# Optimization experiments

Hardware: AMD Instinct MI355X
Metric: run time of the kernel (lower is better)

The kernel has to match this reference:

```python
import jax, jax.numpy as jnp
import numpy as np

B, T, C, H, D, G, V, M = 4, 1024, 768, 12, 4, 4, 32000, 1024
S = C // H


def layernorm(x, g, b, eps=1e-5):
    mu = jnp.mean(x, -1, keepdims=True)
    var = jnp.mean(jnp.square(x - mu), -1, keepdims=True)
    return (x - mu) * jax.lax.rsqrt(var + eps) * g + b


def setup_inputs() -> dict:
    key = jax.random.key(0)
    ks = jax.random.split(key, 12)
    std = 0.02  # matches _init_weights normal(0, 0.02)
    n = lambda k, sh: jax.random.normal(k, sh, jnp.float32) * std
    return {
        'x': jax.random.randint(ks[0], (B, T), 0, V),
        'y': jax.random.randint(ks[1], (B, T), 0, V),
        'wordemb': n(ks[2], (V, C)),
        'posemb': n(ks[3], (M, C)),
        'Wq': n(ks[4], (D, C, C)),
        'Wk': n(ks[5], (D, C, C)),
        'Wv': n(ks[6], (D, C, C)),
        'Wo': n(ks[7], (D, C, C)),
        'bo': jnp.zeros((D, C), jnp.float32),
        'ln1_g': jnp.ones((D, C), jnp.float32),
        'ln1_b': jnp.zeros((D, C), jnp.float32),
        'W1': n(ks[8], (D, C, G * C)),
        'b1': jnp.zeros((D, G * C), jnp.float32),
        'W2': n(ks[9], (D, G * C, C)),
        'b2': jnp.zeros((D, C), jnp.float32),
        'ln2_g': jnp.ones((D, C), jnp.float32),
        'ln2_b': jnp.zeros((D, C), jnp.float32),
        'Wl': n(ks[10], (C, V)),
        'bl': jnp.zeros((V,), jnp.float32),
    }


def _forward(x, y, wordemb, posemb, Wq, Wk, Wv, Wo, bo, ln1_g, ln1_b,
             W1, b1, W2, b2, ln2_g, ln2_b, Wl, bl):
    b, t = x.shape
    emb = wordemb[x] + posemb[:t][None, :, :]  # (b,t,c)
    causal = jnp.tril(jnp.ones((t, t), bool))

    def block(h_in, p):
        wq, wk, wv, wo, bo_, g1, be1, w1, b1_, w2, b2_, g2, be2 = p
        q = (h_in @ wq).reshape(b, t, H, S)
        k = (h_in @ wk).reshape(b, t, H, S)
        v = (h_in @ wv).reshape(b, t, H, S)
        # note: original scales by sqrt(channels), NOT sqrt(head_dim)
        w = jnp.einsum('bqhs,bkhs->bhqk', q, k) / jnp.sqrt(jnp.float32(C))
        w = jnp.where(causal, w, -jnp.inf)
        w = jax.nn.softmax(w, axis=-1)
        att = jnp.einsum('bhqk,bkhs->bqhs', w, v).reshape(b, t, C)
        att = att @ wo + bo_
        h1 = h_in + layernorm(att, g1, be1)   # x + norm1(attn(x))
        ff = jax.nn.relu(h1 @ w1 + b1_) @ w2 + b2_
        h2 = h1 + layernorm(ff, g2, be2)      # x + norm2(ff(x)); dropout=0
        return h2, None

    hfin, _ = jax.lax.scan(
        block, emb,
        (Wq, Wk, Wv, Wo, bo, ln1_g, ln1_b, W1, b1, W2, b2, ln2_g, ln2_b))
    logits = hfin @ Wl + bl  # (b,t,v)
    logp = jax.nn.log_softmax(logits, axis=-1)
    nll = -jnp.take_along_axis(logp, y[..., None], axis=-1)[..., 0]
    loss = jnp.mean(nll)
    return logits, loss


def reference(x, y, wordemb, posemb, Wq, Wk, Wv, Wo, bo, ln1_g, ln1_b,
              W1, b1, W2, b2, ln2_g, ln2_b, Wl, bl):
    return _forward(x, y, wordemb, posemb, Wq, Wk, Wv, Wo, bo, ln1_g, ln1_b,
                    W1, b1, W2, b2, ln2_g, ln2_b, Wl, bl)
```

## Files before the change

kernel.cpp:

```cpp
#include <hip/hip_runtime.h>

#define Bn 4
#define Tn 1024
#define Cn 768
#define Hn 12
#define Dn 4
#define Vn 32000
#define BTn (Bn*Tn)
#define NBX 125

typedef __attribute__((ext_vector_type(8))) short short8;
typedef __attribute__((ext_vector_type(4))) float f32x4;

__device__ __forceinline__ unsigned short f2bf(float f) {
  union { float f; unsigned u; } v; v.f = f;
  unsigned r = v.u + 0x7fffu + ((v.u >> 16) & 1u);
  return (unsigned short)(r >> 16);
}
__device__ __forceinline__ float bf2f(unsigned short us) {
  union { unsigned u; float f; } t; t.u = ((unsigned)us) << 16; return t.f;
}

__device__ __forceinline__ void gload_lds16(const void* g, void* l) {
  __builtin_amdgcn_global_load_lds(
      (const __attribute__((address_space(1))) void*)g,
      (__attribute__((address_space(3))) void*)l, 16, 0, 0);
}

__global__ __launch_bounds__(256)
void transpose_bf16_kernel(const float* __restrict__ src0, unsigned short* __restrict__ dst0,
                           int K, int N, size_t sStride, size_t dStride) {
  const float* src = src0 + blockIdx.z * sStride;
  unsigned short* dst = dst0 + blockIdx.z * dStride;
  __shared__ float tile[32][33];
  const int tx = threadIdx.x, ty = threadIdx.y;
  const int n0 = blockIdx.x * 32, k0 = blockIdx.y * 32;
#pragma unroll
  for (int i = 0; i < 4; ++i)
    tile[ty + i*8][tx] = src[(size_t)(k0 + ty + i*8) * N + n0 + tx];
  __syncthreads();
#pragma unroll
  for (int i = 0; i < 4; ++i)
    dst[(size_t)(n0 + ty + i*8) * K + k0 + tx] = f2bf(tile[tx][ty + i*8]);
}

__global__ __launch_bounds__(256)
void embed_kernel(const int* __restrict__ x, const float* __restrict__ wordemb,
                  const float* __restrict__ posemb, unsigned short* __restrict__ hb) {
  int i4 = blockIdx.x * 256 + threadIdx.x;
  int row = i4 / (Cn/4), c4 = i4 % (Cn/4);
  int t = row & (Tn - 1);
  int tok = x[row];
  float4 a = ((const float4*)wordemb)[(size_t)tok * (Cn/4) + c4];
  float4 p = ((const float4*)posemb)[(size_t)t * (Cn/4) + c4];
  ushort4 u; u.x = f2bf(a.x+p.x); u.y = f2bf(a.y+p.y); u.z = f2bf(a.z+p.z); u.w = f2bf(a.w+p.w);
  ((ushort4*)hb)[i4] = u;
}

__global__ __launch_bounds__(256, 2)
void gemm_l(const unsigned short* __restrict__ A, const unsigned short* __restrict__ Bt,
            const float* __restrict__ bias, float* __restrict__ Cf,
            unsigned short* __restrict__ Cb, int M, int N, int K, int relu,
            unsigned short* __restrict__ vTp) {
  __shared__ __align__(16) unsigned short lds[2*16384];
  const int tid = threadIdx.x;
  const int gx = gridDim.x;
  const int flat = blockIdx.x + gx*blockIdx.y;
  const int chq = (gx * gridDim.y) >> 3;
  const int swz = (flat & 7)*chq + (flat >> 3);
  const int by = swz % gx, bx = swz / gx;
  const int lane = tid & 63, w = tid >> 6;
  const int wr = w >> 1, wc = w & 1;
  const int lr = lane & 15, lq = lane >> 4;
  const int xm = (lr >> 1) & 3;
  const int sslot = (lane & 3) ^ ((lane >> 3) & 3);
  const int NT = K >> 6;

  f32x4 acc[4][4];
#pragma unroll
  for (int i = 0; i < 4; ++i)
#pragma unroll
    for (int j = 0; j < 4; ++j)
      acc[i][j] = (f32x4){0.f, 0.f, 0.f, 0.f};

  const unsigned short* aS = A  + (size_t)(by*128 + w*16 + (lane>>2))*K + sslot*8;
  const unsigned short* bS = Bt + (size_t)(bx*128 + w*16 + (lane>>2))*K + sslot*8;

  auto stA = [&](int t) {
    unsigned short* d = &lds[(t&1)*16384];
    const int k0 = t*64;
#pragma unroll
    for (int kh = 0; kh < 2; ++kh)
#pragma unroll
      for (int i = 0; i < 2; ++i)
        gload_lds16(aS + k0 + kh*32 + (size_t)i*64*K, d + kh*4096 + (i*64 + w*16)*32);
  };
  auto stB = [&](int t) {
    unsigned short* d = &lds[(t&1)*16384 + 8192];
    const int k0 = t*64;
#pragma unroll
    for (int kh = 0; kh < 2; ++kh)
#pragma unroll
      for (int i = 0; i < 2; ++i)
        gload_lds16(bS + k0 + kh*32 + (size_t)i*64*K, d + kh*4096 + (i*64 + w*16)*32);
  };
  auto rdA = [&](int t, int kh, short8* af) {
    const unsigned short* p = &lds[(t&1)*16384 + kh*4096];
#pragma unroll
    for (int mi = 0; mi < 4; ++mi)
      af[mi] = *(const short8*)&p[(wr*64 + mi*16 + lr)*32 + (lq ^ xm)*8];
  };
  auto rdB = [&](int t, int kh, short8* bf) {
    const unsigned short* p = &lds[(t&1)*16384 + 8192 + kh*4096];
#pragma unroll
    for (int nj = 0; nj < 4; ++nj)
      bf[nj] = *(const short8*)&p[(wc*64 + nj*16 + lr)*32 + (lq ^ xm)*8];
  };

  short8 af0[4], af1[4], bf0[4], bf1[4];
  stA(0); stB(0); stA(1);

  for (int t = 0; t < NT; ++t) {
    if (t + 1 < NT) { asm volatile("s_waitcnt vmcnt(4)" ::: "memory"); }
    else            { asm volatile("s_waitcnt vmcnt(0)" ::: "memory"); }
    __builtin_amdgcn_s_barrier();
    __builtin_amdgcn_sched_barrier(0);
    rdA(t, 0, af0); rdA(t, 1, af1); rdB(t, 0, bf0);
    if (t + 1 < NT) stB(t + 1);
    __builtin_amdgcn_s_barrier();
    __builtin_amdgcn_sched_barrier(0);
    __builtin_amdgcn_s_setprio(1);
#pragma unroll
    for (int i = 0; i < 4; ++i)
#pragma unroll
      for (int j = 0; j < 4; ++j)
        acc[i][j] = __builtin_amdgcn_mfma_f32_16x16x32_bf16(af0[i], bf0[j], acc[i][j], 0, 0, 0);
    __builtin_amdgcn_s_setprio(0);
    __builtin_amdgcn_s_barrier();
    rdB(t, 1, bf1);
    if (t + 2 < NT) stA(t + 2);
    __builtin_amdgcn_s_barrier();
    __builtin_amdgcn_sched_barrier(0);
    __builtin_amdgcn_s_setprio(1);
#pragma unroll
    for (int i = 0; i < 4; ++i)
#pragma unroll
      for (int j = 0; j < 4; ++j)
        acc[i][j] = __builtin_amdgcn_mfma_f32_16x16x32_bf16(af1[i], bf1[j], acc[i][j], 0, 0, 0);
    __builtin_amdgcn_s_setprio(0);
  }

  const bool isV = (vTp != nullptr) && (bx*128 >= 1536);
  if (!isV) {
#pragma unroll
    for (int mi = 0; mi < 4; ++mi)
#pragma unroll
      for (int nj = 0; nj < 4; ++nj)
#pragma unroll
        for (int r = 0; r < 4; ++r) {
          int grow = by*128 + wr*64 + mi*16 + lq*4 + r;
          int gcol = bx*128 + wc*64 + nj*16 + lr;
          float v = acc[mi][nj][r];
          if (bias) v += bias[gcol];
          if (relu) v = fmaxf(v, 0.f);
          size_t idx = (size_t)grow * N + gcol;
          if (Cf) Cf[idx] = v;
          if (Cb) Cb[idx] = f2bf(v);
        }
  } else {
    __syncthreads();
    unsigned short (*tile)[136] = (unsigned short (*)[136])lds;
#pragma unroll
    for (int mi = 0; mi < 4; ++mi)
#pragma unroll
      for (int nj = 0; nj < 4; ++nj)
#pragma unroll
        for (int r = 0; r < 4; ++r) {
          int lt = wr*64 + mi*16 + lq*4 + r;
          int ld = wc*64 + nj*16 + lr;
          tile[ld][lt] = f2bf(acc[mi][nj][r]);
        }
    __syncthreads();
    const int bq = (by*128) >> 10;
    const int t0 = (by*128) & 1023;
#pragma unroll
    for (int i = 0; i < 32; ++i) {
      int ld = w*32 + i;
      int gd = bx*128 + ld - 1536;
      int hh2 = gd >> 6, dd = gd & 63;
      ushort2 val = *(ushort2*)&tile[ld][2*lane];
      *(ushort2*)&vTp[((size_t)((bq*Hn + hh2)*64 + dd))*Tn + t0 + 2*lane] = val;
    }
  }
}

__global__ __launch_bounds__(512, 1)
void gemm_vocab(const unsigned short* __restrict__ A, const unsigned short* __restrict__ Bt,
                const float* __restrict__ bias, float* __restrict__ Cf,
                float2* __restrict__ lsepart) {
  constexpr int K = 768, N = Vn, NT = 12;
  __shared__ __align__(16) unsigned short lds[2*32768];
  const int tid = threadIdx.x;
  const int bid = blockIdx.x;
  const int swz = (bid & 7)*250 + (bid >> 3);
  const int by = swz & 15, bx = swz >> 4;
  const int lane = tid & 63, w = tid >> 6;
  const int wr = w >> 2, wc = w & 3;
  const int lr = lane & 15, lq = lane >> 4;
  const int xm = (lr >> 1) & 3;
  const int sslot = (lane & 3) ^ ((lane >> 3) & 3);

  f32x4 accLo[4][4], accHi[4][4];
#pragma unroll
  for (int i = 0; i < 4; ++i)
#pragma unroll
    for (int j = 0; j < 4; ++j) {
      accLo[i][j] = (f32x4){0.f,0.f,0.f,0.f};
      accHi[i][j] = (f32x4){0.f,0.f,0.f,0.f};
    }

  const unsigned short* aS = A  + (size_t)(by*256 + w*16 + (lane>>2))*K + sslot*8;
  const unsigned short* bS = Bt + (size_t)(bx*256 + w*16 + (lane>>2))*K + sslot*8;

  auto stA = [&](int t) {
    unsigned short* d = &lds[(t&1)*32768];
    const int k0 = t*64;
#pragma unroll
    for (int kh = 0; kh < 2; ++kh)
#pragma unroll
      for (int i = 0; i < 2; ++i)
        gload_lds16(aS + k0 + kh*32 + (size_t)i*128*K, d + kh*8192 + (i*128 + w*16)*32);
  };
  auto stB = [&](int t) {
    unsigned short* d = &lds[(t&1)*32768 + 16384];
    const int k0 = t*64;
#pragma unroll
    for (int kh = 0; kh < 2; ++kh)
#pragma unroll
      for (int i = 0; i < 2; ++i)
        gload_lds16(bS + k0 + kh*32 + (size_t)i*128*K, d + kh*8192 + (i*128 + w*16)*32);
  };
  auto rdA = [&](int t, int kh, int mh, short8* af) {
    const unsigned short* p = &lds[(t&1)*32768 + kh*8192];
#pragma unroll
    for (int mi = 0; mi < 4; ++mi)
      af[mi] = *(const short8*)&p[(wr*128 + mh*64 + mi*16 + lr)*32 + (lq ^ xm)*8];
  };
  auto rdB = [&](int t, int kh, short8* bf) {
    const unsigned short* p = &lds[(t&1)*32768 + 16384 + kh*8192];
#pragma unroll
    for (int nj = 0; nj < 4; ++nj)
      bf[nj] = *(const short8*)&p[(wc*64 + nj*16 + lr)*32 + (lq ^ xm)*8];
  };

  short8 aLo0[4], aHi0[4], aLo1[4], aHi1[4], bf0[4], bf1[4];
  stA(0); stB(0); stA(1); stB(1);

  for (int t = 0; t < NT; ++t) {
    if (t + 1 < NT) { asm volatile("s_waitcnt vmcnt(8)" ::: "memory"); }
    else            { asm volatile("s_waitcnt vmcnt(0)" ::: "memory"); }
    __builtin_amdgcn_s_barrier();
    __builtin_amdgcn_sched_barrier(0);
    rdA(t, 0, 0, aLo0); rdA(t, 0, 1, aHi0); rdB(t, 0, bf0);
    __builtin_amdgcn_s_barrier();
    __builtin_amdgcn_sched_barrier(0);
    __builtin_amdgcn_s_setprio(1);
#pragma unroll
    for (int i = 0; i < 4; ++i)
#pragma unroll
      for (int j = 0; j < 4; ++j)
        accLo[i][j] = __builtin_amdgcn_mfma_f32_16x16x32_bf16(aLo0[i], bf0[j], accLo[i][j], 0, 0, 0);
    __builtin_amdgcn_s_setprio(0);
    __builtin_amdgcn_s_barrier();
    rdA(t, 1, 0, aLo1); rdA(t, 1, 1, aHi1);
    __builtin_amdgcn_s_barrier();
    __builtin_amdgcn_sched_barrier(0);
    __builtin_amdgcn_s_setprio(1);
#pragma unroll
    for (int i = 0; i < 4; ++i)
#pragma unroll
      for (int j = 0; j < 4; ++j)
        accHi[i][j] = __builtin_amdgcn_mfma_f32_16x16x32_bf16(aHi0[i], bf0[j], accHi[i][j], 0, 0, 0);
    __builtin_amdgcn_s_setprio(0);
    __builtin_amdgcn_s_barrier();
    rdB(t, 1, bf1);
    if (t + 2 < NT) stA(t + 2);
    __builtin_amdgcn_s_barrier();
    __builtin_amdgcn_sched_barrier(0);
    __builtin_amdgcn_s_setprio(1);
#pragma unroll
    for (int i = 0; i < 4; ++i)
#pragma unroll
      for (int j = 0; j < 4; ++j)
        accLo[i][j] = __builtin_amdgcn_mfma_f32_16x16x32_bf16(aLo1[i], bf1[j], accLo[i][j], 0, 0, 0);
    __builtin_amdgcn_s_setprio(0);
    __builtin_amdgcn_s_barrier();
    if (t + 2 < NT) stB(t + 2);
    __builtin_amdgcn_s_barrier();
    __builtin_amdgcn_sched_barrier(0);
    __builtin_amdgcn_s_setprio(1);
#pragma unroll
    for (int i = 0; i < 4; ++i)
#pragma unroll
      for (int j = 0; j < 4; ++j)
        accHi[i][j] = __builtin_amdgcn_mfma_f32_16x16x32_bf16(aHi1[i], bf1[j], accHi[i][j], 0, 0, 0);
    __builtin_amdgcn_s_setprio(0);
  }

  float2* part = (float2*)lds;
#pragma unroll
  for (int half = 0; half < 2; ++half) {
#pragma unroll
    for (int mi = 0; mi < 4; ++mi)
#pragma unroll
      for (int r = 0; r < 4; ++r) {
        float v[4]; float m = -3.0e38f;
#pragma unroll
        for (int nj = 0; nj < 4; ++nj) {
          int gcol = bx*256 + wc*64 + nj*16 + lr;
          float val = (half ? accHi[mi][nj][r] : accLo[mi][nj][r]) + bias[gcol];
          v[nj] = val;
          m = fmaxf(m, val);
        }
        int prow = wr*128 + half*64 + mi*16 + lq*4 + r;
        int grow = by*256 + prow;
        float* crow = Cf + (size_t)grow * N + bx*256 + wc*64 + lr;
#pragma unroll
        for (int nj = 0; nj < 4; ++nj)
          __builtin_nontemporal_store(v[nj], &crow[nj*16]);
        float s = 0.f;
#pragma unroll
        for (int nj = 0; nj < 4; ++nj) s += __expf(v[nj] - m);
#pragma unroll
        for (int mask = 1; mask < 16; mask <<= 1) {
          float m2 = __shfl_xor(m, mask), s2 = __shfl_xor(s, mask);
          float mn = fmaxf(m, m2);
          s = s*__expf(m - mn) + s2*__expf(m2 - mn);
          m = mn;
        }
        if (lr == 0) part[prow*4 + wc] = make_float2(m, s);
      }
  }
  __syncthreads();
  if (tid < 256) {
    float2 p = part[tid*4];
    float m = p.x, s = p.y;
#pragma unroll
    for (int wcc = 1; wcc < 4; ++wcc) {
      float2 p2 = part[tid*4 + wcc];
      float mn = fmaxf(m, p2.x);
      s = s*__expf(m - mn) + p2.y*__expf(p2.x - mn);
      m = mn;
    }
    lsepart[(size_t)(by*256 + tid)*NBX + bx] = make_float2(m, s);
  }
}

__global__ __launch_bounds__(256)
void attn_mfma_kernel(const unsigned short* __restrict__ qkvb,
                      const unsigned short* __restrict__ vT,
                      unsigned short* __restrict__ attb) {
  const int qb = blockIdx.x, hh = blockIdx.y, b = blockIdx.z;
  const int t = threadIdx.x;
  const int lane = t & 63, w = t >> 6;
  const int lr = lane & 15, lg = lane >> 4;
  const float scale = 0.03608439182435161f;

  __shared__ unsigned short Ks[2][64*64];
  __shared__ unsigned short Vs[2][64*64];
  __shared__ unsigned short Ps[4][16][72];

  const unsigned short* qsrc = qkvb + (size_t)(b*Tn + qb*64 + w*16 + lr)*2304 + hh*64 + lg*8;
  short8 qa0 = *(const short8*)(qsrc);
  short8 qa1 = *(const short8*)(qsrc + 32);

  f32x4 acc[4];
#pragma unroll
  for (int dt = 0; dt < 4; ++dt) acc[dt] = (f32x4){0.f,0.f,0.f,0.f};
  float m_run[4], l_run[4];
#pragma unroll
  for (int r = 0; r < 4; ++r) { m_run[r] = -1e30f; l_run[r] = 0.f; }

  const int sr = t >> 2, c2 = t & 3;

  auto stage = [&](int kvb) {
    const int buf = kvb & 1;
    const unsigned short* ksrc = qkvb + (size_t)(b*Tn + kvb*64 + sr)*2304 + 768 + hh*64 + c2*16;
    short8 k0 = *(const short8*)ksrc;
    short8 k1 = *(const short8*)(ksrc + 8);
    const unsigned short* vsrc = vT + ((size_t)((b*Hn + hh)*64 + sr))*Tn + kvb*64 + c2*16;
    short8 vv0 = *(const short8*)vsrc;
    short8 vv1 = *(const short8*)(vsrc + 8);
    int s0 = (2*c2) ^ (sr & 7), s1 = (2*c2 + 1) ^ (sr & 7);
    *(short8*)&Ks[buf][sr*64 + s0*8] = k0;
    *(short8*)&Ks[buf][sr*64 + s1*8] = k1;
    *(short8*)&Vs[buf][sr*64 + s0*8] = vv0;
    *(short8*)&Vs[buf][sr*64 + s1*8] = vv1;
  };

  stage(0);
  __syncthreads();

  for (int kvb = 0; kvb <= qb; ++kvb) {
    if (kvb < qb) stage(kvb + 1);
    const int buf = kvb & 1;

    f32x4 s[4];
#pragma unroll
    for (int kt = 0; kt < 4; ++kt) {
      int krow = kt*16 + lr;
      short8 kf0 = *(const short8*)&Ks[buf][krow*64 + ((0 + lg) ^ (krow & 7))*8];
      short8 kf1 = *(const short8*)&Ks[buf][krow*64 + ((4 + lg) ^ (krow & 7))*8];
      f32x4 a = (f32x4){0.f,0.f,0.f,0.f};
      a = __builtin_amdgcn_mfma_f32_16x16x32_bf16(qa0, kf0, a, 0, 0, 0);
      a = __builtin_amdgcn_mfma_f32_16x16x32_bf16(qa1, kf1, a, 0, 0, 0);
      s[kt] = a;
    }
    const bool diag = (kvb == qb);
#pragma unroll
    for (int kt = 0; kt < 4; ++kt)
#pragma unroll
      for (int r = 0; r < 4; ++r) {
        float v = s[kt][r] * scale;
        if (diag && (kt*16 + lr > w*16 + lg*4 + r)) v = -1e30f;
        s[kt][r] = v;
      }
#pragma unroll
    for (int r = 0; r < 4; ++r) {
      float m = fmaxf(fmaxf(s[0][r], s[1][r]), fmaxf(s[2][r], s[3][r]));
      m = fmaxf(m, __shfl_xor(m, 1));
      m = fmaxf(m, __shfl_xor(m, 2));
      m = fmaxf(m, __shfl_xor(m, 4));
      m = fmaxf(m, __shfl_xor(m, 8));
      float mn = fmaxf(m_run[r], m);
      float corr = __expf(m_run[r] - mn);
      m_run[r] = mn;
      float ps = 0.f;
#pragma unroll
      for (int kt = 0; kt < 4; ++kt) {
        float p = __expf(s[kt][r] - mn);
        s[kt][r] = p;
        ps += p;
      }
      ps += __shfl_xor(ps, 1);
      ps += __shfl_xor(ps, 2);
      ps += __shfl_xor(ps, 4);
      ps += __shfl_xor(ps, 8);
      l_run[r] = l_run[r] * corr + ps;
#pragma unroll
      for (int dt = 0; dt < 4; ++dt) acc[dt][r] *= corr;
    }
#pragma unroll
    for (int kt = 0; kt < 4; ++kt)
#pragma unroll
      for (int r = 0; r < 4; ++r)
        Ps[w][lg*4 + r][kt*16 + lr] = f2bf(s[kt][r]);
    short8 pa0 = *(const short8*)&Ps[w][lr][lg*8];
    short8 pa1 = *(const short8*)&Ps[w][lr][32 + lg*8];
#pragma unroll
    for (int dt = 0; dt < 4; ++dt) {
      int drow = dt*16 + lr;
      short8 vf0 = *(const short8*)&Vs[buf][drow*64 + ((0 + lg) ^ (drow & 7))*8];
      short8 vf1 = *(const short8*)&Vs[buf][drow*64 + ((4 + lg) ^ (drow & 7))*8];
      acc[dt] = __builtin_amdgcn_mfma_f32_16x16x32_bf16(pa0, vf0, acc[dt], 0, 0, 0);
      acc[dt] = __builtin_amdgcn_mfma_f32_16x16x32_bf16(pa1, vf1, acc[dt], 0, 0, 0);
    }
    __syncthreads();
  }

  unsigned short* obase = attb + (size_t)(b*Tn + qb*64 + w*16)*768 + hh*64;
#pragma unroll
  for (int dt = 0; dt < 4; ++dt)
#pragma unroll
    for (int r = 0; r < 4; ++r) {
      float v = acc[dt][r] / l_run[r];
      obase[(size_t)(lg*4 + r)*768 + dt*16 + lr] = f2bf(v);
    }
}

__global__ __launch_bounds__(256)
void ln_res_kernel(const unsigned short* __restrict__ xb, unsigned short* __restrict__ hb,
                   const float* __restrict__ g, const float* __restrict__ bb) {
  const int lane = threadIdx.x & 63;
  const int row = blockIdx.x*4 + (threadIdx.x >> 6);
  const ushort4* xr4 = (const ushort4*)(xb + (size_t)row * Cn);
  ushort4* hb4 = (ushort4*)(hb + (size_t)row * Cn);
  float4 v[3];
  float s1 = 0.f, s2 = 0.f;
#pragma unroll
  for (int j = 0; j < 3; ++j) {
    ushort4 u = xr4[lane + j*64];
    v[j].x = bf2f(u.x); v[j].y = bf2f(u.y); v[j].z = bf2f(u.z); v[j].w = bf2f(u.w);
    s1 += v[j].x + v[j].y + v[j].z + v[j].w;
    s2 += v[j].x*v[j].x + v[j].y*v[j].y + v[j].z*v[j].z + v[j].w*v[j].w;
  }
#pragma unroll
  for (int m = 1; m < 64; m <<= 1) { s1 += __shfl_xor(s1, m); s2 += __shfl_xor(s2, m); }
  float mu = s1 * (1.f/768.f);
  float var = s2 * (1.f/768.f) - mu*mu;
  float rs = rsqrtf(var + 1e-5f);
  const float4* g4 = (const float4*)g;
  const float4* b4 = (const float4*)bb;
#pragma unroll
  for (int j = 0; j < 3; ++j) {
    int c = lane + j*64;
    ushort4 hu = hb4[c];
    float4 gv = g4[c], bv = b4[c];
    float y0 = bf2f(hu.x) + (v[j].x - mu)*rs*gv.x + bv.x;
    float y1 = bf2f(hu.y) + (v[j].y - mu)*rs*gv.y + bv.y;
    float y2 = bf2f(hu.z) + (v[j].z - mu)*rs*gv.z + bv.z;
    float y3 = bf2f(hu.w) + (v[j].w - mu)*rs*gv.w + bv.w;
    ushort4 u; u.x = f2bf(y0); u.y = f2bf(y1); u.z = f2bf(y2); u.w = f2bf(y3);
    hb4[c] = u;
  }
}

__global__ __launch_bounds__(128)
void loss_part_kernel(const float2* __restrict__ part, const float* __restrict__ logits,
                      const int* __restrict__ y, float* __restrict__ loss_rows) {
  const int row = blockIdx.x, tid = threadIdx.x;
  float m = -3.0e38f, s = 0.f;
  if (tid < NBX) { float2 p = part[(size_t)row*NBX + tid]; m = p.x; s = p.y; }
#pragma unroll
  for (int mask = 1; mask < 64; mask <<= 1) {
    float m2 = __shfl_xor(m, mask), s2 = __shfl_xor(s, mask);
    float mn = fmaxf(m, m2);
    s = s*__expf(m - mn) + s2*__expf(m2 - mn);
    m = mn;
  }
  __shared__ float mw[2], sw[2];
  if ((tid & 63) == 0) { mw[tid >> 6] = m; sw[tid >> 6] = s; }
  __syncthreads();
  if (tid == 0) {
    float m2 = mw[1], s2 = sw[1];
    float mn = fmaxf(m, m2);
    s = s*__expf(m - mn) + s2*__expf(m2 - mn);
    loss_rows[row] = mn + __logf(s) - logits[(size_t)row*Vn + y[row]];
  }
}

__global__ __launch_bounds__(256)
void loss_reduce_kernel(const float* __restrict__ loss_rows, float* __restrict__ out) {
  const int tid = threadIdx.x;
  float s = 0.f;
  for (int j = 0; j < BTn/256; ++j) s += loss_rows[tid + j*256];
  __shared__ float red[256];
  red[tid] = s; __syncthreads();
  for (int st = 128; st > 0; st >>= 1) {
    if (tid < st) red[tid] += red[tid+st];
    __syncthreads();
  }
  if (tid == 0) out[0] = red[0] * (1.f/(float)BTn);
}

extern "C" void kernel_launch(void* const* d_in, const int* in_sizes, int n_in,
                              void* d_out, int out_size, void* d_ws, size_t ws_size,
                              hipStream_t stream) {
  const int*   x       = (const int*)  d_in[0];
  const int*   y       = (const int*)  d_in[1];
  const float* wordemb = (const float*)d_in[2];
  const float* posemb  = (const float*)d_in[3];
  const float* Wq      = (const float*)d_in[4];
  const float* Wk      = (const float*)d_in[5];
  const float* Wv      = (const float*)d_in[6];
  const float* Wo      = (const float*)d_in[7];
  const float* bo      = (const float*)d_in[8];
  const float* ln1_g   = (const float*)d_in[9];
  const float* ln1_b   = (const float*)d_in[10];
  const float* W1      = (const float*)d_in[11];
  const float* b1      = (const float*)d_in[12];
  const float* W2      = (const float*)d_in[13];
  const float* b2      = (const float*)d_in[14];
  const float* ln2_g   = (const float*)d_in[15];
  const float* ln2_b   = (const float*)d_in[16];
  const float* Wl      = (const float*)d_in[17];
  const float* bl      = (const float*)d_in[18];

  char* ws = (char*)d_ws;
  size_t off = 0;
  auto alloc = [&](size_t bytes) -> char* {
    char* p = ws + off;
    off += (bytes + 255) & ~(size_t)255;
    return p;
  };
  unsigned short* wqkvT = (unsigned short*)alloc((size_t)Dn*2304*768*2);
  unsigned short* woT   = (unsigned short*)alloc((size_t)Dn*768*768*2);
  unsigned short* w1T   = (unsigned short*)alloc((size_t)Dn*3072*768*2);
  unsigned short* w2T   = (unsigned short*)alloc((size_t)Dn*768*3072*2);
  unsigned short* wlT   = (unsigned short*)alloc((size_t)Vn*768*2);
  unsigned short* hb    = (unsigned short*)alloc((size_t)BTn*Cn*2);
  unsigned short* qkvb  = (unsigned short*)alloc((size_t)BTn*3072*2);
  unsigned short* vTb   = (unsigned short*)alloc((size_t)Bn*Hn*64*Tn*2);
  unsigned short* attb  = (unsigned short*)alloc((size_t)BTn*Cn*2);
  unsigned short* tmpb  = (unsigned short*)alloc((size_t)BTn*Cn*2);
  float*          loss_rows = (float*)alloc((size_t)BTn*4);
  float2*         lsepart   = (float2*)alloc((size_t)BTn*NBX*8);
  unsigned short* ff1b  = qkvb;

  dim3 tb(32, 8);
  transpose_bf16_kernel<<<dim3(24,24,Dn), tb, 0, stream>>>(Wq, wqkvT,             Cn, Cn, (size_t)Cn*Cn, (size_t)2304*768);
  transpose_bf16_kernel<<<dim3(24,24,Dn), tb, 0, stream>>>(Wk, wqkvT + 768*768,   Cn, Cn, (size_t)Cn*Cn, (size_t)2304*768);
  transpose_bf16_kernel<<<dim3(24,24,Dn), tb, 0, stream>>>(Wv, wqkvT + 1536*768,  Cn, Cn, (size_t)Cn*Cn, (size_t)2304*768);
  transpose_bf16_kernel<<<dim3(24,24,Dn), tb, 0, stream>>>(Wo, woT,               Cn, Cn, (size_t)Cn*Cn, (size_t)768*768);
  transpose_bf16_kernel<<<dim3(96,24,Dn), tb, 0, stream>>>(W1, w1T, 768, 3072, (size_t)768*3072, (size_t)3072*768);
  transpose_bf16_kernel<<<dim3(24,96,Dn), tb, 0, stream>>>(W2, w2T, 3072, 768, (size_t)3072*768, (size_t)768*3072);
  transpose_bf16_kernel<<<dim3(1000,24,1), tb, 0, stream>>>(Wl, wlT, 768, Vn, 0, 0);

  embed_kernel<<<(BTn*Cn/4)/256, 256, 0, stream>>>(x, wordemb, posemb, hb);

  for (int d = 0; d < Dn; ++d) {
    gemm_l<<<dim3(BTn/128, 2304/128), 256, 0, stream>>>(
        hb, wqkvT + (size_t)d*2304*768, nullptr, nullptr, qkvb, BTn, 2304, 768, 0, vTb);
    attn_mfma_kernel<<<dim3(Tn/64, Hn, Bn), 256, 0, stream>>>(qkvb, vTb, attb);
    gemm_l<<<dim3(BTn/128, 768/128), 256, 0, stream>>>(
        attb, woT + (size_t)d*768*768, bo + (size_t)d*768, nullptr, tmpb, BTn, 768, 768, 0, nullptr);
    ln_res_kernel<<<BTn/4, 256, 0, stream>>>(tmpb, hb, ln1_g + (size_t)d*768, ln1_b + (size_t)d*768);
    gemm_l<<<dim3(BTn/128, 3072/128), 256, 0, stream>>>(
        hb, w1T + (size_t)d*3072*768, b1 + (size_t)d*3072, nullptr, ff1b, BTn, 3072, 768, 1, nullptr);
    gemm_l<<<dim3(BTn/128, 768/128), 256, 0, stream>>>(
        ff1b, w2T + (size_t)d*768*3072, b2 + (size_t)d*768, nullptr, tmpb, BTn, 768, 3072, 0, nullptr);
    ln_res_kernel<<<BTn/4, 256, 0, stream>>>(tmpb, hb, ln2_g + (size_t)d*768, ln2_b + (size_t)d*768);
  }

  float* logits = (float*)d_out;
  gemm_vocab<<<2000, 512, 0, stream>>>(hb, wlT, bl, logits, lsepart);
  loss_part_kernel<<<BTn, 128, 0, stream>>>(lsepart, logits, y, loss_rows);
  loss_reduce_kernel<<<1, 256, 0, stream>>>(loss_rows, logits + (size_t)BTn*Vn);
}
```

Before: 1.208 ms.

## Process two 64-key tiles per iteration in causal attention kernel

```diff
diff --git a/kernel.cpp b/kernel.cpp
--- a/kernel.cpp
+++ b/kernel.cpp
@@ -366,8 +366,8 @@
   const int lr = lane & 15, lg = lane >> 4;
   const float scale = 0.03608439182435161f;
 
-  __shared__ unsigned short Ks[2][64*64];
-  __shared__ unsigned short Vs[2][64*64];
+  __shared__ unsigned short Ks[2][128*64];
+  __shared__ unsigned short Vs[2][64*128];
   __shared__ unsigned short Ps[4][16][72];
 
   const unsigned short* qsrc = qkvb + (size_t)(b*Tn + qb*64 + w*16 + lr)*2304 + hh*64 + lg*8;
@@ -381,53 +381,70 @@
 #pragma unroll
   for (int r = 0; r < 4; ++r) { m_run[r] = -1e30f; l_run[r] = 0.f; }
 
-  const int sr = t >> 2, c2 = t & 3;
-
-  auto stage = [&](int kvb) {
-    const int buf = kvb & 1;
-    const unsigned short* ksrc = qkvb + (size_t)(b*Tn + kvb*64 + sr)*2304 + 768 + hh*64 + c2*16;
-    short8 k0 = *(const short8*)ksrc;
-    short8 k1 = *(const short8*)(ksrc + 8);
-    const unsigned short* vsrc = vT + ((size_t)((b*Hn + hh)*64 + sr))*Tn + kvb*64 + c2*16;
-    short8 vv0 = *(const short8*)vsrc;
-    short8 vv1 = *(const short8*)(vsrc + 8);
-    int s0 = (2*c2) ^ (sr & 7), s1 = (2*c2 + 1) ^ (sr & 7);
-    *(short8*)&Ks[buf][sr*64 + s0*8] = k0;
-    *(short8*)&Ks[buf][sr*64 + s1*8] = k1;
-    *(short8*)&Vs[buf][sr*64 + s0*8] = vv0;
-    *(short8*)&Vs[buf][sr*64 + s1*8] = vv1;
+  const int NT2 = (qb >> 1) + 1;
+  const int kr = t >> 1, khalf = t & 1;
+  const int vr = t >> 2, vq = t & 3;
+
+  auto stage = [&](int kv2) {
+    const int buf = kv2 & 1;
+    const unsigned short* ksrc = qkvb + (size_t)(b*Tn + kv2*128 + kr)*2304 + 768 + hh*64 + khalf*32;
+#pragma unroll
+    for (int j = 0; j < 4; ++j) {
+      short8 kv = *(const short8*)(ksrc + j*8);
+      int phys = (khalf*4 + j) ^ (kr & 7);
+      *(short8*)&Ks[buf][kr*64 + phys*8] = kv;
+    }
+    const unsigned short* vsrc = vT + ((size_t)((b*Hn + hh)*64 + vr))*Tn + kv2*128 + vq*32;
+#pragma unroll
+    for (int j = 0; j < 4; ++j) {
+      short8 vv = *(const short8*)(vsrc + j*8);
+      int sl = vq*4 + j;
+      int phys = (sl & 8) | ((sl & 7) ^ (vr & 7));
+      *(short8*)&Vs[buf][vr*128 + phys*8] = vv;
+    }
   };
 
   stage(0);
   __syncthreads();
 
-  for (int kvb = 0; kvb <= qb; ++kvb) {
-    if (kvb < qb) stage(kvb + 1);
-    const int buf = kvb & 1;
-
-    f32x4 s[4];
-#pragma unroll
-    for (int kt = 0; kt < 4; ++kt) {
-      int krow = kt*16 + lr;
-      short8 kf0 = *(const short8*)&Ks[buf][krow*64 + ((0 + lg) ^ (krow & 7))*8];
-      short8 kf1 = *(const short8*)&Ks[buf][krow*64 + ((4 + lg) ^ (krow & 7))*8];
-      f32x4 a = (f32x4){0.f,0.f,0.f,0.f};
-      a = __builtin_amdgcn_mfma_f32_16x16x32_bf16(qa0, kf0, a, 0, 0, 0);
-      a = __builtin_amdgcn_mfma_f32_16x16x32_bf16(qa1, kf1, a, 0, 0, 0);
-      s[kt] = a;
-    }
-    const bool diag = (kvb == qb);
+  for (int kv2 = 0; kv2 < NT2; ++kv2) {
+    if (kv2 + 1 < NT2) stage(kv2 + 1);
+    const int buf = kv2 & 1;
+    const int t0 = 2*kv2, t1 = 2*kv2 + 1;
+    const bool do1 = (t1 <= qb);
+
+    f32x4 s0[4], s1[4];
+#pragma unroll
+    for (int sub = 0; sub < 2; ++sub) {
+      if (sub == 1 && !do1) break;
+      f32x4* ss = sub ? s1 : s0;
+#pragma unroll
+      for (int kt = 0; kt < 4; ++kt) {
+        int krow = sub*64 + kt*16 + lr;
+        short8 kf0 = *(const short8*)&Ks[buf][krow*64 + ((0 + lg) ^ (krow & 7))*8];
+        short8 kf1 = *(const short8*)&Ks[buf][krow*64 + ((4 + lg) ^ (krow & 7))*8];
+        f32x4 a = (f32x4){0.f,0.f,0.f,0.f};
+        a = __builtin_amdgcn_mfma_f32_16x16x32_bf16(qa0, kf0, a, 0, 0, 0);
+        a = __builtin_amdgcn_mfma_f32_16x16x32_bf16(qa1, kf1, a, 0, 0, 0);
+        ss[kt] = a;
+      }
+    }
+    const bool dg0 = (t0 == qb), dg1 = (t1 == qb);
 #pragma unroll
     for (int kt = 0; kt < 4; ++kt)
 #pragma unroll
       for (int r = 0; r < 4; ++r) {
-        float v = s[kt][r] * scale;
-        if (diag && (kt*16 + lr > w*16 + lg*4 + r)) v = -1e30f;
-        s[kt][r] = v;
+        float v0 = s0[kt][r] * scale;
+        if (dg0 && (kt*16 + lr > w*16 + lg*4 + r)) v0 = -1e30f;
+        s0[kt][r] = v0;
+        float v1 = do1 ? s1[kt][r] * scale : -1e30f;
+        if (dg1 && (kt*16 + lr > w*16 + lg*4 + r)) v1 = -1e30f;
+        s1[kt][r] = v1;
       }
 #pragma unroll
     for (int r = 0; r < 4; ++r) {
-      float m = fmaxf(fmaxf(s[0][r], s[1][r]), fmaxf(s[2][r], s[3][r]));
+      float m = fmaxf(fmaxf(fmaxf(s0[0][r], s0[1][r]), fmaxf(s0[2][r], s0[3][r])),
+                      fmaxf(fmaxf(s1[0][r], s1[1][r]), fmaxf(s1[2][r], s1[3][r])));
       m = fmaxf(m, __shfl_xor(m, 1));
       m = fmaxf(m, __shfl_xor(m, 2));
       m = fmaxf(m, __shfl_xor(m, 4));
@@ -438,9 +455,8 @@
       float ps = 0.f;
 #pragma unroll
       for (int kt = 0; kt < 4; ++kt) {
-        float p = __expf(s[kt][r] - mn);
-        s[kt][r] = p;
-        ps += p;
+        float p0 = __expf(s0[kt][r] - mn); s0[kt][r] = p0; ps += p0;
+        float p1 = __expf(s1[kt][r] - mn); s1[kt][r] = p1; ps += p1;
       }
       ps += __shfl_xor(ps, 1);
       ps += __shfl_xor(ps, 2);
@@ -454,16 +470,35 @@
     for (int kt = 0; kt < 4; ++kt)
 #pragma unroll
       for (int r = 0; r < 4; ++r)
-        Ps[w][lg*4 + r][kt*16 + lr] = f2bf(s[kt][r]);
-    short8 pa0 = *(const short8*)&Ps[w][lr][lg*8];
-    short8 pa1 = *(const short8*)&Ps[w][lr][32 + lg*8];
-#pragma unroll
-    for (int dt = 0; dt < 4; ++dt) {
-      int drow = dt*16 + lr;
-      short8 vf0 = *(const short8*)&Vs[buf][drow*64 + ((0 + lg) ^ (drow & 7))*8];
-      short8 vf1 = *(const short8*)&Vs[buf][drow*64 + ((4 + lg) ^ (drow & 7))*8];
-      acc[dt] = __builtin_amdgcn_mfma_f32_16x16x32_bf16(pa0, vf0, acc[dt], 0, 0, 0);
-      acc[dt] = __builtin_amdgcn_mfma_f32_16x16x32_bf16(pa1, vf1, acc[dt], 0, 0, 0);
+        Ps[w][lg*4 + r][kt*16 + lr] = f2bf(s0[kt][r]);
+    {
+      short8 pa0 = *(const short8*)&Ps[w][lr][lg*8];
+      short8 pa1 = *(const short8*)&Ps[w][lr][32 + lg*8];
+#pragma unroll
+      for (int dt = 0; dt < 4; ++dt) {
+        int drow = dt*16 + lr;
+        short8 vf0 = *(const short8*)&Vs[buf][drow*128 + ((0 + lg) ^ (drow & 7))*8];
+        short8 vf1 = *(const short8*)&Vs[buf][drow*128 + ((4 + lg) ^ (drow & 7))*8];
+        acc[dt] = __builtin_amdgcn_mfma_f32_16x16x32_bf16(pa0, vf0, acc[dt], 0, 0, 0);
+        acc[dt] = __builtin_amdgcn_mfma_f32_16x16x32_bf16(pa1, vf1, acc[dt], 0, 0, 0);
+      }
+    }
+    if (do1) {
+#pragma unroll
+      for (int kt = 0; kt < 4; ++kt)
+#pragma unroll
+        for (int r = 0; r < 4; ++r)
+          Ps[w][lg*4 + r][kt*16 + lr] = f2bf(s1[kt][r]);
+      short8 pa0 = *(const short8*)&Ps[w][lr][lg*8];
+      short8 pa1 = *(const short8*)&Ps[w][lr][32 + lg*8];
+#pragma unroll
+      for (int dt = 0; dt < 4; ++dt) {
+        int drow = dt*16 + lr;
+        short8 vf0 = *(const short8*)&Vs[buf][drow*128 + (8 + ((0 + lg) ^ (drow & 7)))*8];
+        short8 vf1 = *(const short8*)&Vs[buf][drow*128 + (8 + ((4 + lg) ^ (drow & 7)))*8];
+        acc[dt] = __builtin_amdgcn_mfma_f32_16x16x32_bf16(pa0, vf0, acc[dt], 0, 0, 0);
+        acc[dt] = __builtin_amdgcn_mfma_f32_16x16x32_bf16(pa1, vf1, acc[dt], 0, 0, 0);
+      }
     }
     __syncthreads();
   }
```

Result: slower. 1.237 ms (+2.4%).

## Split-K the N=768 projection GEMMs and fuse partial sums into layernorm

Applied to the files above, without the earlier changes.

```diff
diff --git a/kernel.cpp b/kernel.cpp
--- a/kernel.cpp
+++ b/kernel.cpp
@@ -60,11 +60,12 @@
 __global__ __launch_bounds__(256, 2)
 void gemm_l(const unsigned short* __restrict__ A, const unsigned short* __restrict__ Bt,
             const float* __restrict__ bias, float* __restrict__ Cf,
-            unsigned short* __restrict__ Cb, int M, int N, int K, int relu,
+            unsigned short* __restrict__ Cb, int M, int N, int K, int KLD, int relu,
             unsigned short* __restrict__ vTp) {
   __shared__ __align__(16) unsigned short lds[2*16384];
   const int tid = threadIdx.x;
   const int gx = gridDim.x;
+  const int kz = blockIdx.z;
   const int flat = blockIdx.x + gx*blockIdx.y;
   const int chq = (gx * gridDim.y) >> 3;
   const int swz = (flat & 7)*chq + (flat >> 3);
@@ -83,8 +84,8 @@
     for (int j = 0; j < 4; ++j)
       acc[i][j] = (f32x4){0.f, 0.f, 0.f, 0.f};
 
-  const unsigned short* aS = A  + (size_t)(by*128 + w*16 + (lane>>2))*K + sslot*8;
-  const unsigned short* bS = Bt + (size_t)(bx*128 + w*16 + (lane>>2))*K + sslot*8;
+  const unsigned short* aS = A  + (size_t)(by*128 + w*16 + (lane>>2))*KLD + kz*K + sslot*8;
+  const unsigned short* bS = Bt + (size_t)(bx*128 + w*16 + (lane>>2))*KLD + kz*K + sslot*8;
 
   auto stA = [&](int t) {
     unsigned short* d = &lds[(t&1)*16384];
@@ -93,7 +94,7 @@
     for (int kh = 0; kh < 2; ++kh)
 #pragma unroll
       for (int i = 0; i < 2; ++i)
-        gload_lds16(aS + k0 + kh*32 + (size_t)i*64*K, d + kh*4096 + (i*64 + w*16)*32);
+        gload_lds16(aS + k0 + kh*32 + (size_t)i*64*KLD, d + kh*4096 + (i*64 + w*16)*32);
   };
   auto stB = [&](int t) {
     unsigned short* d = &lds[(t&1)*16384 + 8192];
@@ -102,7 +103,7 @@
     for (int kh = 0; kh < 2; ++kh)
 #pragma unroll
       for (int i = 0; i < 2; ++i)
-        gload_lds16(bS + k0 + kh*32 + (size_t)i*64*K, d + kh*4096 + (i*64 + w*16)*32);
+        gload_lds16(bS + k0 + kh*32 + (size_t)i*64*KLD, d + kh*4096 + (i*64 + w*16)*32);
   };
   auto rdA = [&](int t, int kh, short8* af) {
     const unsigned short* p = &lds[(t&1)*16384 + kh*4096];
@@ -152,6 +153,7 @@
 
   const bool isV = (vTp != nullptr) && (bx*128 >= 1536);
   if (!isV) {
+    const size_t zoff = (size_t)kz * M * N;
 #pragma unroll
     for (int mi = 0; mi < 4; ++mi)
 #pragma unroll
@@ -161,10 +163,10 @@
           int grow = by*128 + wr*64 + mi*16 + lq*4 + r;
           int gcol = bx*128 + wc*64 + nj*16 + lr;
           float v = acc[mi][nj][r];
-          if (bias) v += bias[gcol];
+          if (bias && kz == 0) v += bias[gcol];
           if (relu) v = fmaxf(v, 0.f);
           size_t idx = (size_t)grow * N + gcol;
-          if (Cf) Cf[idx] = v;
+          if (Cf) Cf[zoff + idx] = v;
           if (Cb) Cb[idx] = f2bf(v);
         }
   } else {
@@ -491,6 +493,44 @@
   for (int j = 0; j < 3; ++j) {
     ushort4 u = xr4[lane + j*64];
     v[j].x = bf2f(u.x); v[j].y = bf2f(u.y); v[j].z = bf2f(u.z); v[j].w = bf2f(u.w);
+    s1 += v[j].x + v[j].y + v[j].z + v[j].w;
+    s2 += v[j].x*v[j].x + v[j].y*v[j].y + v[j].z*v[j].z + v[j].w*v[j].w;
+  }
+#pragma unroll
+  for (int m = 1; m < 64; m <<= 1) { s1 += __shfl_xor(s1, m); s2 += __shfl_xor(s2, m); }
+  float mu = s1 * (1.f/768.f);
+  float var = s2 * (1.f/768.f) - mu*mu;
+  float rs = rsqrtf(var + 1e-5f);
+  const float4* g4 = (const float4*)g;
+  const float4* b4 = (const float4*)bb;
+#pragma unroll
+  for (int j = 0; j < 3; ++j) {
+    int c = lane + j*64;
+    ushort4 hu = hb4[c];
+    float4 gv = g4[c], bv = b4[c];
+    float y0 = bf2f(hu.x) + (v[j].x - mu)*rs*gv.x + bv.x;
+    float y1 = bf2f(hu.y) + (v[j].y - mu)*rs*gv.y + bv.y;
+    float y2 = bf2f(hu.z) + (v[j].z - mu)*rs*gv.z + bv.z;
+    float y3 = bf2f(hu.w) + (v[j].w - mu)*rs*gv.w + bv.w;
+    ushort4 u; u.x = f2bf(y0); u.y = f2bf(y1); u.z = f2bf(y2); u.w = f2bf(y3);
+    hb4[c] = u;
+  }
+}
+
+__global__ __launch_bounds__(256)
+void ln_res2_kernel(const float* __restrict__ part, unsigned short* __restrict__ hb,
+                    const float* __restrict__ g, const float* __restrict__ bb) {
+  const int lane = threadIdx.x & 63;
+  const int row = blockIdx.x*4 + (threadIdx.x >> 6);
+  const float4* p0 = (const float4*)(part + (size_t)row * Cn);
+  const float4* p1 = (const float4*)(part + (size_t)BTn * Cn + (size_t)row * Cn);
+  ushort4* hb4 = (ushort4*)(hb + (size_t)row * Cn);
+  float4 v[3];
+  float s1 = 0.f, s2 = 0.f;
+#pragma unroll
+  for (int j = 0; j < 3; ++j) {
+    float4 a = p0[lane + j*64], b = p1[lane + j*64];
+    v[j].x = a.x + b.x; v[j].y = a.y + b.y; v[j].z = a.z + b.z; v[j].w = a.w + b.w;
     s1 += v[j].x + v[j].y + v[j].z + v[j].w;
     s2 += v[j].x*v[j].x + v[j].y*v[j].y + v[j].z*v[j].z + v[j].w*v[j].w;
   }
@@ -592,7 +632,7 @@
   unsigned short* qkvb  = (unsigned short*)alloc((size_t)BTn*3072*2);
   unsigned short* vTb   = (unsigned short*)alloc((size_t)Bn*Hn*64*Tn*2);
   unsigned short* attb  = (unsigned short*)alloc((size_t)BTn*Cn*2);
-  unsigned short* tmpb  = (unsigned short*)alloc((size_t)BTn*Cn*2);
+  float*          partf = (float*)alloc((size_t)2*BTn*Cn*4);
   float*          loss_rows = (float*)alloc((size_t)BTn*4);
   float2*         lsepart   = (float2*)alloc((size_t)BTn*NBX*8);
   unsigned short* ff1b  = qkvb;
@@ -610,16 +650,16 @@
 
   for (int d = 0; d < Dn; ++d) {
     gemm_l<<<dim3(BTn/128, 2304/128), 256, 0, stream>>>(
-        hb, wqkvT + (size_t)d*2304*768, nullptr, nullptr, qkvb, BTn, 2304, 768, 0, vTb);
+        hb, wqkvT + (size_t)d*2304*768, nullptr, nullptr, qkvb, BTn, 2304, 768, 768, 0, vTb);
     attn_mfma_kernel<<<dim3(Tn/64, Hn, Bn), 256, 0, stream>>>(qkvb, vTb, attb);
-    gemm_l<<<dim3(BTn/128, 768/128), 256, 0, stream>>>(
-        attb, woT + (size_t)d*768*768, bo + (size_t)d*768, nullptr, tmpb, BTn, 768, 768, 0, nullptr);
-    ln_res_kernel<<<BTn/4, 256, 0, stream>>>(tmpb, hb, ln1_g + (size_t)d*768, ln1_b + (size_t)d*768);
+    gemm_l<<<dim3(BTn/128, 768/128, 2), 256, 0, stream>>>(
+        attb, woT + (size_t)d*768*768, bo + (size_t)d*768, partf, nullptr, BTn, 768, 384, 768, 0, nullptr);
+    ln_res2_kernel<<<BTn/4, 256, 0, stream>>>(partf, hb, ln1_g + (size_t)d*768, ln1_b + (size_t)d*768);
     gemm_l<<<dim3(BTn/128, 3072/128), 256, 0, stream>>>(
-        hb, w1T + (size_t)d*3072*768, b1 + (size_t)d*3072, nullptr, ff1b, BTn, 3072, 768, 1, nullptr);
-    gemm_l<<<dim3(BTn/128, 768/128), 256, 0, stream>>>(
-        ff1b, w2T + (size_t)d*768*3072, b2 + (size_t)d*768, nullptr, tmpb, BTn, 768, 3072, 0, nullptr);
-    ln_res_kernel<<<BTn/4, 256, 0, stream>>>(tmpb, hb, ln2_g + (size_t)d*768, ln2_b + (size_t)d*768);
+        hb, w1T + (size_t)d*3072*768, b1 + (size_t)d*3072, nullptr, ff1b, BTn, 3072, 768, 768, 1, nullptr);
+    gemm_l<<<dim3(BTn/128, 768/128, 2), 256, 0, stream>>>(
+        ff1b, w2T + (size_t)d*768*3072, b2 + (size_t)d*768, partf, nullptr, BTn, 768, 1536, 3072, 0, nullptr);
+    ln_res2_kernel<<<BTn/4, 256, 0, stream>>>(partf, hb, ln2_g + (size_t)d*768, ln2_b + (size_t)d*768);
   }
 
   float* logits = (float*)d_out;
```

Measured after the change: 1.188 ms. About the same (-1.7%).
